# Performance work log

Measured on AMD Instinct MI355X. Metric: run time of the kernel, lower is better.

Reference implementation:

```python
import jax, jax.numpy as jnp
import numpy as np

# Dims: B=2, T=4 -> BT=8 frames; S=H*W=256 tokens/frame; L=25 stacked LLM layers; D=4096 llm hidden
BT, S, L, D = 8, 256, 25, 4096
C, NH = 1024, 8          # teacher_hid_size (hard-coded), num_heads
HD = C // NH             # 128
LAYER_IDX = np.array([24, 20, 16, 12, 8, 4, 0])  # num_layer=24 - arange(0,25,4)
J = len(LAYER_IDX)       # 7 distillation layers
SCALE = C ** -0.5        # NOTE: teacher_hid_size**-0.5, NOT head_dim**-0.5 (faithful to source)
EPS_LN, EPS_COS = 1e-5, 1e-8


def setup_inputs() -> dict:
    key = jax.random.key(0)
    ks = jax.random.split(key, 7)
    def n(k, shape, s=1.0):
        return jax.random.normal(k, shape, dtype=jnp.float32) * s
    return {
        "all_features": n(ks[0], (BT, S, L, D)),
        "teacher_features": n(ks[1], (BT, S, C)),
        "ln_gamma": jnp.ones((J, D), jnp.float32),
        "ln_beta": jnp.zeros((J, D), jnp.float32),
        "norm_w": n(ks[2], (J, C, D), 0.02),   # per-layer Linear(llm->teacher), no bias
        "input_w": n(ks[3], (C, D), 0.02),
        "input_b": n(ks[4], (C,), 0.02),
        "output_w": n(ks[5], (C, C), 0.02),
        "output_b": n(ks[6], (C,), 0.02),
    }


def reference(all_features, teacher_features, ln_gamma, ln_beta, norm_w,
              input_w, input_b, output_w, output_b):
    # Gather the distilled layers: [BT, S, J, D]
    x = all_features[:, :, LAYER_IDX]
    # Per-layer LayerNorm (each norm_layer[j] has its own affine params)
    mu = x.mean(-1, keepdims=True)
    var = ((x - mu) ** 2).mean(-1, keepdims=True)
    xn = (x - mu) * jax.lax.rsqrt(var + EPS_LN) * ln_gamma + ln_beta
    # Per-layer Linear (bias=False): stack -> vision_outputs [BT, S, J, C]
    vo = jnp.einsum('bsjd,jcd->bsjc', xn, norm_w)
    # input_layer on last hidden state: vision_input [BT, S, C]
    vin = jnp.einsum('bsd,cd->bsc', all_features[:, :, -1], input_w) + input_b
    # Hand-rolled multiplicative cross-attention over the J layer axis
    voh = vo.reshape(BT, S, J, NH, HD)
    q = voh[:, :, 0]        # [BT, S, NH, HD]
    kv = voh[:, :, 1:]      # [BT, S, J-1, NH, HD]
    scores = jnp.einsum('bshd,bskhd->bshk', q * SCALE, kv)   # [BT, S, NH, J-1]
    attn = jax.nn.softmax(scores, axis=-1)
    fuse = jnp.einsum('bshk,bskhd->bshd', attn, kv).reshape(BT, S, C)
    vf = vin + jnp.einsum('bsc,oc->bso', fuse, output_w) + output_b  # vision_feature
    # Cosine distillation loss vs teacher (torch CosineSimilarity eps=1e-8)
    na = jnp.maximum(jnp.linalg.norm(vf, axis=-1), EPS_COS)
    nb = jnp.maximum(jnp.linalg.norm(teacher_features, axis=-1), EPS_COS)
    cos = (vf * teacher_features).sum(-1) / (na * nb)        # [BT, S]
    # sum_i (1 - mean_s cos_i) / count_image, count_image = BT  ->  1 - mean over all
    return 1.0 - cos.mean()
```

## Files before the change

### kernel.cpp

```cpp
#include <hip/hip_runtime.h>
#include <cstdint>
#include <cstring>

#define M_TOK 2048
#define DDIM 4096
#define CDIM 1024
#define LTOT 25

typedef __bf16 bf16_t;
typedef __attribute__((ext_vector_type(8))) __bf16 bf16x8;
typedef __attribute__((ext_vector_type(4))) float f32x4;
typedef __attribute__((ext_vector_type(16))) float f32x16;
typedef __attribute__((ext_vector_type(8))) int i32x8;
typedef __attribute__((ext_vector_type(4))) unsigned int u32x4;
typedef unsigned char u8;

__device__ __forceinline__ void gload16(const void* g, void* l) {
  __builtin_amdgcn_global_load_lds(
      (const __attribute__((address_space(1))) unsigned int*)g,
      (__attribute__((address_space(3))) unsigned int*)l, 16, 0, 0);
}

__device__ __forceinline__ unsigned int pk4_fp8(float x, float y, float z, float w) {
  int r = __builtin_amdgcn_cvt_pk_fp8_f32(x, y, 0, false);
  r = __builtin_amdgcn_cvt_pk_fp8_f32(z, w, r, true);
  return (unsigned int)r;
}

__device__ __forceinline__ u8 f32_to_fp8(float x) {
  return (u8)(__builtin_amdgcn_cvt_pk_fp8_f32(x, 0.f, 0, false) & 0xff);
}

__device__ __forceinline__ float fp8_to_f32(u8 b) {
  return __builtin_amdgcn_cvt_f32_fp8((int)b, 0);
}

__global__ void cvt_fp8(const float* __restrict__ src, u8* __restrict__ dst, long n) {
  long stride = (long)gridDim.x * blockDim.x;
  for (long i = (long)blockIdx.x * blockDim.x + threadIdx.x; i * 8 < n; i += stride) {
    const float4* s4 = (const float4*)(src + i * 8);
    float4 a = s4[0], b = s4[1];
    uint2 pk;
    pk.x = pk4_fp8(a.x, a.y, a.z, a.w);
    pk.y = pk4_fp8(b.x, b.y, b.z, b.w);
    *(uint2*)(dst + i * 8) = pk;
  }
}

__global__ void cvt_bf16(const float* __restrict__ src, bf16_t* __restrict__ dst, long n) {
  long stride = (long)gridDim.x * blockDim.x;
  for (long i = (long)blockIdx.x * blockDim.x + threadIdx.x; i * 8 < n; i += stride) {
    const float4* s4 = (const float4*)(src + i * 8);
    float4 a = s4[0], b = s4[1];
    bf16_t o[8] = {(bf16_t)a.x, (bf16_t)a.y, (bf16_t)a.z, (bf16_t)a.w,
                   (bf16_t)b.x, (bf16_t)b.y, (bf16_t)b.z, (bf16_t)b.w};
    uint4 pk;
    __builtin_memcpy(&pk, o, 16);
    *(uint4*)(dst + i * 8) = pk;
  }
}

__global__ __launch_bounds__(256)
void ln_convert(const float* __restrict__ af, const float* __restrict__ gamma,
                const float* __restrict__ beta, u8* __restrict__ xn,
                int jBase, int fuse7)
{
  int m = blockIdx.x;
  int jl = blockIdx.y;
  int j = jBase + jl;
  int layer = (j < 7) ? (24 - 4 * j) : 24;
  const float4* row4 = (const float4*)(af + ((size_t)m * LTOT + layer) * DDIM);
  int tid = threadIdx.x;
  float4 v[4];
  float s = 0.f, ss = 0.f;
#pragma unroll
  for (int i = 0; i < 4; ++i) {
    v[i] = row4[i * 256 + tid];
    s += v[i].x + v[i].y + v[i].z + v[i].w;
    ss += v[i].x * v[i].x + v[i].y * v[i].y + v[i].z * v[i].z + v[i].w * v[i].w;
  }
  int lane = tid & 63, wv = tid >> 6;
#pragma unroll
  for (int off = 32; off; off >>= 1) { s += __shfl_xor(s, off); ss += __shfl_xor(ss, off); }
  __shared__ float red[8];
  if (lane == 0) { red[wv] = s; red[4 + wv] = ss; }
  __syncthreads();
  s = red[0] + red[1] + red[2] + red[3];
  ss = red[4] + red[5] + red[6] + red[7];
  float mu = 0.f, rs = 1.f;
  if (j < 7) {
    mu = s * (1.f / DDIM);
    float var = ss * (1.f / DDIM) - mu * mu;
    rs = rsqrtf(var + 1e-5f);
  }
  if (fuse7 && jl == 0) {
    u8* o7 = xn + ((size_t)7 * M_TOK + m) * DDIM;
#pragma unroll
    for (int i = 0; i < 4; ++i)
      ((unsigned int*)o7)[i * 256 + tid] = pk4_fp8(v[i].x, v[i].y, v[i].z, v[i].w);
  }
  u8* orow = xn + ((size_t)jl * M_TOK + m) * DDIM;
  int jw = (j < 7) ? j : 0;
  const float4* g4 = (const float4*)(gamma + (size_t)jw * DDIM);
  const float4* b4 = (const float4*)(beta + (size_t)jw * DDIM);
#pragma unroll
  for (int i = 0; i < 4; ++i) {
    float4 x = v[i];
    float4 ov;
    if (j < 7) {
      float4 g = g4[i * 256 + tid], bb = b4[i * 256 + tid];
      ov.x = (x.x - mu) * rs * g.x + bb.x;
      ov.y = (x.y - mu) * rs * g.y + bb.y;
      ov.z = (x.z - mu) * rs * g.z + bb.z;
      ov.w = (x.w - mu) * rs * g.w + bb.w;
    } else ov = x;
    ((unsigned int*)orow)[i * 256 + tid] = pk4_fp8(ov.x, ov.y, ov.z, ov.w);
  }
}

__global__ __launch_bounds__(256)
void prep(const float* __restrict__ af, const float* __restrict__ gamma,
          const float* __restrict__ beta, u8* __restrict__ xn,
          const float* __restrict__ norm_w, const float* __restrict__ input_w,
          const float* __restrict__ output_w, u8* __restrict__ wb8,
          bf16_t* __restrict__ owb)
{
  int tid = threadIdx.x;
  if (blockIdx.y == 7) {
    const long NW7 = (long)7 * CDIM * DDIM;
    const long NWI = (long)8 * CDIM * DDIM;
    const long TOT = NWI + (long)CDIM * CDIM;
    long stride = (long)gridDim.x * blockDim.x;
    for (long i = (long)blockIdx.x * blockDim.x + tid; i * 8 < TOT; i += stride) {
      long e = i * 8;
      const float* sp;
      if (e < NW7)      sp = norm_w + e;
      else if (e < NWI) sp = input_w + (e - NW7);
      else              sp = output_w + (e - NWI);
      const float4* s4 = (const float4*)sp;
      float4 a = s4[0], b = s4[1];
      if (e < NWI) {
        uint2 pk;
        pk.x = pk4_fp8(a.x, a.y, a.z, a.w);
        pk.y = pk4_fp8(b.x, b.y, b.z, b.w);
        *(uint2*)(wb8 + e) = pk;
      } else {
        bf16_t o[8] = {(bf16_t)a.x, (bf16_t)a.y, (bf16_t)a.z, (bf16_t)a.w,
                       (bf16_t)b.x, (bf16_t)b.y, (bf16_t)b.z, (bf16_t)b.w};
        uint4 pk;
        __builtin_memcpy(&pk, o, 16);
        *(uint4*)(owb + (e - NWI)) = pk;
      }
    }
    return;
  }
  int m = blockIdx.x;
  int jl = blockIdx.y;
  int layer = 24 - 4 * jl;
  const float4* row4 = (const float4*)(af + ((size_t)m * LTOT + layer) * DDIM);
  float4 v[4];
  float s = 0.f, ss = 0.f;
#pragma unroll
  for (int i = 0; i < 4; ++i) {
    v[i] = row4[i * 256 + tid];
    s += v[i].x + v[i].y + v[i].z + v[i].w;
    ss += v[i].x * v[i].x + v[i].y * v[i].y + v[i].z * v[i].z + v[i].w * v[i].w;
  }
  int lane = tid & 63, wv = tid >> 6;
#pragma unroll
  for (int off = 32; off; off >>= 1) { s += __shfl_xor(s, off); ss += __shfl_xor(ss, off); }
  __shared__ float red[8];
  if (lane == 0) { red[wv] = s; red[4 + wv] = ss; }
  __syncthreads();
  s = red[0] + red[1] + red[2] + red[3];
  ss = red[4] + red[5] + red[6] + red[7];
  float mu = s * (1.f / DDIM);
  float var = ss * (1.f / DDIM) - mu * mu;
  float rs = rsqrtf(var + 1e-5f);
  if (jl == 0) {
    u8* o7 = xn + ((size_t)7 * M_TOK + m) * DDIM;
#pragma unroll
    for (int i = 0; i < 4; ++i)
      ((unsigned int*)o7)[i * 256 + tid] = pk4_fp8(v[i].x, v[i].y, v[i].z, v[i].w);
  }
  u8* orow = xn + ((size_t)jl * M_TOK + m) * DDIM;
  const float4* g4 = (const float4*)(gamma + (size_t)jl * DDIM);
  const float4* b4 = (const float4*)(beta + (size_t)jl * DDIM);
#pragma unroll
  for (int i = 0; i < 4; ++i) {
    float4 x = v[i];
    float4 g = g4[i * 256 + tid], bb = b4[i * 256 + tid];
    float4 ov;
    ov.x = (x.x - mu) * rs * g.x + bb.x;
    ov.y = (x.y - mu) * rs * g.y + bb.y;
    ov.z = (x.z - mu) * rs * g.z + bb.z;
    ov.w = (x.w - mu) * rs * g.w + bb.w;
    ((unsigned int*)orow)[i * 256 + tid] = pk4_fp8(ov.x, ov.y, ov.z, ov.w);
  }
}

__global__ __launch_bounds__(512, 2)
void gemm256mx(const u8* __restrict__ A, const u8* __restrict__ B,
               u8* __restrict__ vo8, bf16_t* __restrict__ vinB,
               const float* __restrict__ bias,
               int Mm, int Nn, int Kk, int jBase, int tilesPerJ, int tilesN)
{
  __shared__ __align__(16) u8 smem[131072];
  int nb = gridDim.x;
  int bid = blockIdx.x;
  if ((nb & 7) == 0) { int cpx = nb >> 3; bid = (bid & 7) * cpx + (bid >> 3); }
  int jl = bid / tilesPerJ;
  int t0 = bid % tilesPerJ;
  int bm = t0 / tilesN, bn = t0 % tilesN;
  int jg = jBase + jl;

  const u8* Aj = A + (size_t)jl * Mm * Kk + (size_t)bm * 256 * Kk;
  const u8* Bj = B + (size_t)jl * Nn * Kk + (size_t)bn * 256 * Kk;

  int tid = threadIdx.x;
  int lane = tid & 63, wid = tid >> 6;
  int wm = wid >> 2, wn = wid & 3;

  int S = wid * 64 + lane;
  int ib_s = S >> 7;
  int s2 = S & 127;
  int lh_s = s2 >> 6;
  int s3 = s2 & 63;
  int l31_s = s3 >> 1;
  int hs = s3 & 1;
  int h_s = hs ^ ((l31_s >> 2) & 1);
  int row_s = ib_s * 32 + l31_s;
  int koff_s = lh_s * 32 + h_s * 16;
  const u8* AsrcC0 = Aj + (size_t)row_s * Kk + koff_s;
  const u8* AsrcC1 = Aj + (size_t)(128 + row_s) * Kk + koff_s;
  const u8* BsrcC0 = Bj + (size_t)row_s * Kk + koff_s;
  const u8* BsrcC1 = Bj + (size_t)(128 + row_s) * Kk + koff_s;

  int l31 = lane & 31;
  int lh = lane >> 5;
  int x16 = ((l31 >> 2) & 1) << 4;
  int loOff = lh * 1024 + l31 * 32 + x16;
  int hiOff = lh * 1024 + l31 * 32 + (16 ^ x16);
  int bBlk = (wn >> 1) * 8192 + ((wn & 1) * 2) * 2048;

  int NT = Kk >> 6;
  f32x16 acc[4][2] = {};

#define STAGE4(tt_)                                                              \
  { gload16(AsrcC0 + (size_t)(tt_) * 64, &smem[((tt_) & 3) * 16384 + wid * 1024]); \
    gload16(AsrcC1 + (size_t)(tt_) * 64, &smem[((tt_) & 3) * 16384 + 8192 + wid * 1024]); \
    gload16(BsrcC0 + (size_t)(tt_) * 64, &smem[65536 + ((tt_) & 3) * 16384 + wid * 1024]); \
    gload16(BsrcC1 + (size_t)(tt_) * 64, &smem[65536 + ((tt_) & 3) * 16384 + 8192 + wid * 1024]); }

#define BAR() asm volatile("s_barrier" ::: "memory")

  STAGE4(0);
  if (NT > 1) STAGE4(1);
  if (NT > 2) STAGE4(2);
  if (NT > 2)      asm volatile("s_waitcnt vmcnt(8)" ::: "memory");
  else if (NT > 1) asm volatile("s_waitcnt vmcnt(4)" ::: "memory");
  else             asm volatile("s_waitcnt vmcnt(0)" ::: "memory");
  BAR();

#pragma unroll 1
  for (int t = 0; t < NT; ++t) {
    const u8* Ab = &smem[(t & 3) * 16384 + wm * 8192];
    const u8* Bb = &smem[65536 + (t & 3) * 16384 + bBlk];
    i32x8 Afr[4], Bfr[2];
#pragma unroll
    for (int ib = 0; ib < 4; ++ib) {
      u32x4 lo = *(const u32x4*)(Ab + ib * 2048 + loOff);
      u32x4 hi = *(const u32x4*)(Ab + ib * 2048 + hiOff);
      Afr[ib][0] = lo[0]; Afr[ib][1] = lo[1]; Afr[ib][2] = lo[2]; Afr[ib][3] = lo[3];
      Afr[ib][4] = hi[0]; Afr[ib][5] = hi[1]; Afr[ib][6] = hi[2]; Afr[ib][7] = hi[3];
    }
#pragma unroll
    for (int jb = 0; jb < 2; ++jb) {
      u32x4 lo = *(const u32x4*)(Bb + jb * 2048 + loOff);
      u32x4 hi = *(const u32x4*)(Bb + jb * 2048 + hiOff);
      Bfr[jb][0] = lo[0]; Bfr[jb][1] = lo[1]; Bfr[jb][2] = lo[2]; Bfr[jb][3] = lo[3];
      Bfr[jb][4] = hi[0]; Bfr[jb][5] = hi[1]; Bfr[jb][6] = hi[2]; Bfr[jb][7] = hi[3];
    }
    if (t + 3 < NT) STAGE4(t + 3);
    __builtin_amdgcn_s_setprio(1);
#pragma unroll
    for (int ib = 0; ib < 4; ++ib)
#pragma unroll
      for (int jb = 0; jb < 2; ++jb)
        acc[ib][jb] = __builtin_amdgcn_mfma_scale_f32_32x32x64_f8f6f4(
            Afr[ib], Bfr[jb], acc[ib][jb], 0, 0, 0, 127, 0, 127);
    __builtin_amdgcn_s_setprio(0);
    if (t + 1 < NT) {
      asm volatile("s_waitcnt lgkmcnt(0)" ::: "memory");
      if (t + 3 < NT)      asm volatile("s_waitcnt vmcnt(8)" ::: "memory");
      else if (t + 2 < NT) asm volatile("s_waitcnt vmcnt(4)" ::: "memory");
      else                 asm volatile("s_waitcnt vmcnt(0)" ::: "memory");
      BAR();
    }
  }
#undef STAGE4
#undef BAR

  int col0 = bn * 256 + wn * 64 + l31;
  int row0 = bm * 256 + wm * 128 + lh * 4;
  if (jg == 7) {
    float bv0 = bias[col0];
    float bv1 = bias[col0 + 32];
#pragma unroll
    for (int ib = 0; ib < 4; ++ib) {
#pragma unroll
      for (int jb = 0; jb < 2; ++jb) {
        float bv = jb ? bv1 : bv0;
        int gc = col0 + jb * 32;
#pragma unroll
        for (int reg = 0; reg < 16; ++reg) {
          int gr = row0 + ib * 32 + (reg & 3) + 8 * (reg >> 2);
          vinB[(size_t)gr * Nn + gc] = (bf16_t)(acc[ib][jb][reg] + bv);
        }
      }
    }
  } else {
    u8* Cj = vo8 + (size_t)jg * Mm * Nn;
#pragma unroll
    for (int ib = 0; ib < 4; ++ib) {
#pragma unroll
      for (int jb = 0; jb < 2; ++jb) {
        int gc = col0 + jb * 32;
#pragma unroll
        for (int reg = 0; reg < 16; ++reg) {
          int gr = row0 + ib * 32 + (reg & 3) + 8 * (reg >> 2);
          Cj[(size_t)gr * Nn + gc] = f32_to_fp8(acc[ib][jb][reg]);
        }
      }
    }
  }
}

__global__ __launch_bounds__(256)
void gemm_bt_epi(const bf16_t* __restrict__ A, const bf16_t* __restrict__ B,
                 float* __restrict__ Cout, const float* __restrict__ bias,
                 const bf16_t* __restrict__ vin, int Mm, int Nn, int Kk, int tilesN)
{
  __shared__ bf16_t As[128 * 64];
  __shared__ bf16_t Bs[128 * 64];
  int bid = blockIdx.x;
  int bm = bid / tilesN, bn = bid % tilesN;
  const bf16_t* Aj = A + (size_t)bm * 128 * Kk;
  const bf16_t* Bj = B + (size_t)bn * 128 * Kk;

  int tid = threadIdx.x;
  int lane = tid & 63, wv = tid >> 6;
  int wm = wv >> 1, wn = wv & 1;

  f32x4 acc[4][4] = {};

  int srow = wv * 32 + (lane >> 3);
  int scol = (lane & 7) * 8;
  const bf16_t* Ag = Aj + (size_t)srow * Kk + scol;
  const bf16_t* Bg = Bj + (size_t)srow * Kk + scol;

  for (int kt = 0; kt < Kk; kt += 64) {
#pragma unroll
    for (int c = 0; c < 4; ++c) {
      gload16(Ag + kt + (size_t)(c * 8) * Kk, &As[(wv * 32 + c * 8) * 64]);
      gload16(Bg + kt + (size_t)(c * 8) * Kk, &Bs[(wv * 32 + c * 8) * 64]);
    }
    __syncthreads();
#pragma unroll
    for (int ks = 0; ks < 2; ++ks) {
      int ko = ks * 32 + (lane >> 4) * 8;
      bf16x8 af[4], bfr[4];
#pragma unroll
      for (int i = 0; i < 4; ++i) {
        af[i] = *(const bf16x8*)&As[(wm * 64 + i * 16 + (lane & 15)) * 64 + ko];
        bfr[i] = *(const bf16x8*)&Bs[(wn * 64 + i * 16 + (lane & 15)) * 64 + ko];
      }
#pragma unroll
      for (int i = 0; i < 4; ++i)
#pragma unroll
        for (int j2 = 0; j2 < 4; ++j2)
          acc[i][j2] = __builtin_amdgcn_mfma_f32_16x16x32_bf16(af[i], bfr[j2], acc[i][j2], 0, 0, 0);
    }
    __syncthreads();
  }

  int rowBase = bm * 128 + wm * 64 + (lane >> 4) * 4;
  int colBase = bn * 128 + wn * 64 + (lane & 15);
#pragma unroll
  for (int i = 0; i < 4; ++i) {
#pragma unroll
    for (int j2 = 0; j2 < 4; ++j2) {
      int gn = colBase + j2 * 16;
      float bv = bias[gn];
#pragma unroll
      for (int r = 0; r < 4; ++r) {
        int gm = rowBase + i * 16 + r;
        Cout[(size_t)gm * Nn + gn] = acc[i][j2][r] + bv + (float)vin[(size_t)gm * Nn + gn];
      }
    }
  }
}

__global__ __launch_bounds__(512)
void attn_fuse(const u8* __restrict__ vo8, bf16_t* __restrict__ fuse)
{
  int m = blockIdx.x;
  int h = threadIdx.x >> 6;
  int lane = threadIdx.x & 63;
  const size_t slab = (size_t)M_TOK * CDIM;
  const u8* base = vo8 + (size_t)m * CDIM + h * 128;
  float q0 = fp8_to_f32(base[lane]), q1 = fp8_to_f32(base[lane + 64]);
  float kv0[6], kv1[6], sc[6];
#pragma unroll
  for (int k = 0; k < 6; ++k) {
    const u8* kb = base + (size_t)(k + 1) * slab;
    kv0[k] = fp8_to_f32(kb[lane]); kv1[k] = fp8_to_f32(kb[lane + 64]);
    sc[k] = q0 * kv0[k] + q1 * kv1[k];
  }
#pragma unroll
  for (int k = 0; k < 6; ++k) {
#pragma unroll
    for (int off = 32; off; off >>= 1) sc[k] += __shfl_xor(sc[k], off);
    sc[k] *= 0.03125f;
  }
  float mx = sc[0];
#pragma unroll
  for (int k = 1; k < 6; ++k) mx = fmaxf(mx, sc[k]);
  float e[6], se = 0.f;
#pragma unroll
  for (int k = 0; k < 6; ++k) { e[k] = expf(sc[k] - mx); se += e[k]; }
  float inv = 1.f / se;
  float f0 = 0.f, f1 = 0.f;
#pragma unroll
  for (int k = 0; k < 6; ++k) { float w = e[k] * inv; f0 += w * kv0[k]; f1 += w * kv1[k]; }
  bf16_t* o = fuse + (size_t)m * CDIM + h * 128;
  o[lane] = (bf16_t)f0;
  o[lane + 64] = (bf16_t)f1;
}

__global__ __launch_bounds__(256)
void cos_row(const float* __restrict__ vf, const float* __restrict__ teacher, float* __restrict__ cosv)
{
  int m = blockIdx.x;
  int tid = threadIdx.x;
  float4 a = ((const float4*)(vf + (size_t)m * CDIM))[tid];
  float4 b = ((const float4*)(teacher + (size_t)m * CDIM))[tid];
  float dot = a.x * b.x + a.y * b.y + a.z * b.z + a.w * b.w;
  float na = a.x * a.x + a.y * a.y + a.z * a.z + a.w * a.w;
  float nb = b.x * b.x + b.y * b.y + b.z * b.z + b.w * b.w;
  int lane = tid & 63, wv = tid >> 6;
#pragma unroll
  for (int off = 32; off; off >>= 1) {
    dot += __shfl_xor(dot, off); na += __shfl_xor(na, off); nb += __shfl_xor(nb, off);
  }
  __shared__ float red[12];
  if (lane == 0) { red[wv] = dot; red[4 + wv] = na; red[8 + wv] = nb; }
  __syncthreads();
  if (tid == 0) {
    float d = red[0] + red[1] + red[2] + red[3];
    float x = red[4] + red[5] + red[6] + red[7];
    float y = red[8] + red[9] + red[10] + red[11];
    float den = fmaxf(sqrtf(x), 1e-8f) * fmaxf(sqrtf(y), 1e-8f);
    cosv[m] = d / den;
  }
}

__global__ __launch_bounds__(256)
void final_reduce(const float* __restrict__ cosv, float* __restrict__ out)
{
  int tid = threadIdx.x;
  float s = 0.f;
  for (int i = tid; i < M_TOK; i += 256) s += cosv[i];
  int lane = tid & 63, wv = tid >> 6;
#pragma unroll
  for (int off = 32; off; off >>= 1) s += __shfl_xor(s, off);
  __shared__ float red[4];
  if (lane == 0) red[wv] = s;
  __syncthreads();
  if (tid == 0) out[0] = 1.f - (red[0] + red[1] + red[2] + red[3]) * (1.f / M_TOK);
}

extern "C" void kernel_launch(void* const* d_in, const int* in_sizes, int n_in,
                              void* d_out, int out_size, void* d_ws, size_t ws_size,
                              hipStream_t stream)
{
  (void)in_sizes; (void)n_in; (void)out_size;
  const float* all_features = (const float*)d_in[0];
  const float* teacher = (const float*)d_in[1];
  const float* ln_gamma = (const float*)d_in[2];
  const float* ln_beta = (const float*)d_in[3];
  const float* norm_w = (const float*)d_in[4];
  const float* input_w = (const float*)d_in[5];
  const float* input_b = (const float*)d_in[6];
  const float* output_w = (const float*)d_in[7];
  const float* output_b = (const float*)d_in[8];
  float* out = (float*)d_out;
  char* ws = (char*)d_ws;

  const size_t M = M_TOK, D = DDIM, C = CDIM;
  const size_t xnB = 8 * M * D;
  const size_t wbB = 8 * C * D;
  const size_t owbB = C * C * 2;
  const size_t vo8B = 7 * M * C;
  const size_t vinB_ = M * C * 2;
  const size_t fuseB = M * C * 2;
  const size_t vfB = M * C * 4;
  const size_t cosB = M * 4;
  const size_t fastTotal = xnB + wbB + owbB + vo8B + vinB_ + fuseB + vfB + cosB;

  if (ws_size >= fastTotal) {
    u8* xn = (u8*)ws;
    u8* wb = (u8*)(ws + xnB);
    bf16_t* owb = (bf16_t*)(ws + xnB + wbB);
    u8* vo8 = (u8*)(ws + xnB + wbB + owbB);
    bf16_t* vinp = (bf16_t*)(ws + xnB + wbB + owbB + vo8B);
    bf16_t* fuse = (bf16_t*)(ws + xnB + wbB + owbB + vo8B + vinB_);
    float* vf = (float*)(ws + xnB + wbB + owbB + vo8B + vinB_ + fuseB);
    float* cosv = (float*)(ws + xnB + wbB + owbB + vo8B + vinB_ + fuseB + vfB);

    dim3 gp((unsigned)M, 8);
    prep<<<gp, 256, 0, stream>>>(all_features, ln_gamma, ln_beta, xn,
                                 norm_w, input_w, output_w, wb, owb);
    gemm256mx<<<256, 512, 0, stream>>>(xn, wb, vo8, vinp, input_b,
                                       (int)M, (int)C, (int)D, 0, 32, 4);
    attn_fuse<<<(unsigned)M, 512, 0, stream>>>(vo8, fuse);
    gemm_bt_epi<<<128, 256, 0, stream>>>(fuse, owb, vf, output_b, vinp,
                                         (int)M, (int)C, (int)C, 8);
    cos_row<<<(unsigned)M, 256, 0, stream>>>(vf, teacher, cosv);
    final_reduce<<<1, 256, 0, stream>>>(cosv, out);
  } else {
    const size_t xn1B = M * D;
    const size_t wb1B = C * D;
    u8* xn1 = (u8*)ws;
    u8* wb1 = (u8*)(ws + xn1B);
    bf16_t* owb = (bf16_t*)(ws + xn1B + wb1B);
    u8* vo8 = (u8*)(ws + xn1B + wb1B + owbB);
    bf16_t* vinp = (bf16_t*)(ws + xn1B + wb1B + owbB + vo8B);
    bf16_t* fuse = (bf16_t*)(ws + xn1B + wb1B + owbB + vo8B + vinB_);
    float* vf = (float*)(ws + xn1B + wb1B + owbB + vo8B + vinB_ + fuseB);
    float* cosv = (float*)(ws + xn1B + wb1B + owbB + vo8B + vinB_ + fuseB + vfB);

    cvt_bf16<<<512, 256, 0, stream>>>(output_w, owb, (long)(C * C));
    for (int j = 0; j < 8; ++j) {
      const float* wsrc = (j < 7) ? (norm_w + (size_t)j * C * D) : input_w;
      cvt_fp8<<<2048, 256, 0, stream>>>(wsrc, wb1, (long)(C * D));
      dim3 g1((unsigned)M, 1);
      ln_convert<<<g1, 256, 0, stream>>>(all_features, ln_gamma, ln_beta, xn1, j, 0);
      gemm256mx<<<32, 512, 0, stream>>>(xn1, wb1, vo8, vinp, input_b,
                                        (int)M, (int)C, (int)D, j, 32, 4);
    }
    attn_fuse<<<(unsigned)M, 512, 0, stream>>>(vo8, fuse);
    gemm_bt_epi<<<128, 256, 0, stream>>>(fuse, owb, vf, output_b, vinp,
                                         (int)M, (int)C, (int)C, 8);
    cos_row<<<(unsigned)M, 256, 0, stream>>>(vf, teacher, cosv);
    final_reduce<<<1, 256, 0, stream>>>(cosv, out);
  }
}
```

Measured before the change: 205.8 us.

## Switch FP8 GEMM to K=128 double-buffered tiles with XOR-swizzled LDS rows

The FP8 MFMA GEMM now loads 128-wide K tiles into two LDS buffers instead of 64-wide tiles into a 4-deep ring. Global-to-LDS loads use a row-major layout with an XOR swizzle on 16-byte chunks to avoid bank conflicts, and each tile runs two MFMA sub-steps. This halves the number of barriers and makes each global load fetch longer contiguous row segments. The cost is shallower prefetch (one tile ahead, with a full vmcnt(0) wait each iteration), which may expose more memory latency.

```diff
diff --git a/kernel.cpp b/kernel.cpp
--- a/kernel.cpp
+++ b/kernel.cpp
@@ -221,84 +221,91 @@
   int lane = tid & 63, wid = tid >> 6;
   int wm = wid >> 2, wn = wid & 3;
 
-  int S = wid * 64 + lane;
-  int ib_s = S >> 7;
-  int s2 = S & 127;
-  int lh_s = s2 >> 6;
-  int s3 = s2 & 63;
-  int l31_s = s3 >> 1;
-  int hs = s3 & 1;
-  int h_s = hs ^ ((l31_s >> 2) & 1);
-  int row_s = ib_s * 32 + l31_s;
-  int koff_s = lh_s * 32 + h_s * 16;
-  const u8* AsrcC0 = Aj + (size_t)row_s * Kk + koff_s;
-  const u8* AsrcC1 = Aj + (size_t)(128 + row_s) * Kk + koff_s;
-  const u8* BsrcC0 = Bj + (size_t)row_s * Kk + koff_s;
-  const u8* BsrcC1 = Bj + (size_t)(128 + row_s) * Kk + koff_s;
+  const u8* AsrcP[4];
+  const u8* BsrcP[4];
+  int AdOff[4], BdOff[4];
+  int pre = ((lane & 7) ^ ((lane >> 3) & 7)) * 16;
+#pragma unroll
+  for (int c = 0; c < 4; ++c) {
+    int S = wid * 4 + c;
+    int chunk = S >> 4, s16 = S & 15;
+    int row = chunk * 128 + s16 * 8 + (lane >> 3);
+    AsrcP[c] = Aj + (size_t)row * Kk + pre;
+    BsrcP[c] = Bj + (size_t)row * Kk + pre;
+    AdOff[c] = chunk * 16384 + s16 * 1024;
+    BdOff[c] = 32768 + chunk * 16384 + s16 * 1024;
+  }
 
   int l31 = lane & 31;
   int lh = lane >> 5;
-  int x16 = ((l31 >> 2) & 1) << 4;
-  int loOff = lh * 1024 + l31 * 32 + x16;
-  int hiOff = lh * 1024 + l31 * 32 + (16 ^ x16);
-  int bBlk = (wn >> 1) * 8192 + ((wn & 1) * 2) * 2048;
-
-  int NT = Kk >> 6;
+  int xk = l31 & 7;
+  int o0[2], o1[2];
+#pragma unroll
+  for (int s = 0; s < 2; ++s) {
+    o0[s] = ((s * 4 + lh * 2) ^ xk) * 16;
+    o1[s] = ((s * 4 + lh * 2 + 1) ^ xk) * 16;
+  }
+  int aRow = l31 * 128;
+  int bRowBase = (wn & 1) * 8192 + l31 * 128;
+  int aChunkOff = wm * 16384;
+  int bChunkOff = 32768 + (wn >> 1) * 16384;
+
+  int NT = Kk >> 7;
   f32x16 acc[4][2] = {};
 
-#define STAGE4(tt_)                                                              \
-  { gload16(AsrcC0 + (size_t)(tt_) * 64, &smem[((tt_) & 3) * 16384 + wid * 1024]); \
-    gload16(AsrcC1 + (size_t)(tt_) * 64, &smem[((tt_) & 3) * 16384 + 8192 + wid * 1024]); \
-    gload16(BsrcC0 + (size_t)(tt_) * 64, &smem[65536 + ((tt_) & 3) * 16384 + wid * 1024]); \
-    gload16(BsrcC1 + (size_t)(tt_) * 64, &smem[65536 + ((tt_) & 3) * 16384 + 8192 + wid * 1024]); }
+#define STAGE2(tt_, bf_)                                                         \
+  { _Pragma("unroll")                                                            \
+    for (int c_ = 0; c_ < 4; ++c_)                                               \
+      gload16(AsrcP[c_] + (size_t)(tt_) * 128, &smem[(bf_) * 65536 + AdOff[c_]]); \
+    _Pragma("unroll")                                                            \
+    for (int c_ = 0; c_ < 4; ++c_)                                               \
+      gload16(BsrcP[c_] + (size_t)(tt_) * 128, &smem[(bf_) * 65536 + BdOff[c_]]); }
 
 #define BAR() asm volatile("s_barrier" ::: "memory")
 
-  STAGE4(0);
-  if (NT > 1) STAGE4(1);
-  if (NT > 2) STAGE4(2);
-  if (NT > 2)      asm volatile("s_waitcnt vmcnt(8)" ::: "memory");
-  else if (NT > 1) asm volatile("s_waitcnt vmcnt(4)" ::: "memory");
-  else             asm volatile("s_waitcnt vmcnt(0)" ::: "memory");
+  STAGE2(0, 0);
+  asm volatile("s_waitcnt vmcnt(0)" ::: "memory");
   BAR();
 
 #pragma unroll 1
   for (int t = 0; t < NT; ++t) {
-    const u8* Ab = &smem[(t & 3) * 16384 + wm * 8192];
-    const u8* Bb = &smem[65536 + (t & 3) * 16384 + bBlk];
-    i32x8 Afr[4], Bfr[2];
-#pragma unroll
-    for (int ib = 0; ib < 4; ++ib) {
-      u32x4 lo = *(const u32x4*)(Ab + ib * 2048 + loOff);
-      u32x4 hi = *(const u32x4*)(Ab + ib * 2048 + hiOff);
-      Afr[ib][0] = lo[0]; Afr[ib][1] = lo[1]; Afr[ib][2] = lo[2]; Afr[ib][3] = lo[3];
-      Afr[ib][4] = hi[0]; Afr[ib][5] = hi[1]; Afr[ib][6] = hi[2]; Afr[ib][7] = hi[3];
-    }
-#pragma unroll
-    for (int jb = 0; jb < 2; ++jb) {
-      u32x4 lo = *(const u32x4*)(Bb + jb * 2048 + loOff);
-      u32x4 hi = *(const u32x4*)(Bb + jb * 2048 + hiOff);
-      Bfr[jb][0] = lo[0]; Bfr[jb][1] = lo[1]; Bfr[jb][2] = lo[2]; Bfr[jb][3] = lo[3];
-      Bfr[jb][4] = hi[0]; Bfr[jb][5] = hi[1]; Bfr[jb][6] = hi[2]; Bfr[jb][7] = hi[3];
-    }
-    if (t + 3 < NT) STAGE4(t + 3);
-    __builtin_amdgcn_s_setprio(1);
-#pragma unroll
-    for (int ib = 0; ib < 4; ++ib)
-#pragma unroll
-      for (int jb = 0; jb < 2; ++jb)
-        acc[ib][jb] = __builtin_amdgcn_mfma_scale_f32_32x32x64_f8f6f4(
-            Afr[ib], Bfr[jb], acc[ib][jb], 0, 0, 0, 127, 0, 127);
-    __builtin_amdgcn_s_setprio(0);
+    int bf = t & 1;
+    if (t + 1 < NT) STAGE2(t + 1, bf ^ 1);
+    const u8* Ac = &smem[bf * 65536 + aChunkOff];
+    const u8* Bc = &smem[bf * 65536 + bChunkOff];
+#pragma unroll
+    for (int s = 0; s < 2; ++s) {
+      i32x8 Afr[4], Bfr[2];
+#pragma unroll
+      for (int ib = 0; ib < 4; ++ib) {
+        u32x4 lo = *(const u32x4*)(Ac + ib * 4096 + aRow + o0[s]);
+        u32x4 hi = *(const u32x4*)(Ac + ib * 4096 + aRow + o1[s]);
+        Afr[ib][0] = lo[0]; Afr[ib][1] = lo[1]; Afr[ib][2] = lo[2]; Afr[ib][3] = lo[3];
+        Afr[ib][4] = hi[0]; Afr[ib][5] = hi[1]; Afr[ib][6] = hi[2]; Afr[ib][7] = hi[3];
+      }
+#pragma unroll
+      for (int jb = 0; jb < 2; ++jb) {
+        u32x4 lo = *(const u32x4*)(Bc + bRowBase + jb * 4096 + o0[s]);
+        u32x4 hi = *(const u32x4*)(Bc + bRowBase + jb * 4096 + o1[s]);
+        Bfr[jb][0] = lo[0]; Bfr[jb][1] = lo[1]; Bfr[jb][2] = lo[2]; Bfr[jb][3] = lo[3];
+        Bfr[jb][4] = hi[0]; Bfr[jb][5] = hi[1]; Bfr[jb][6] = hi[2]; Bfr[jb][7] = hi[3];
+      }
+      __builtin_amdgcn_s_setprio(1);
+#pragma unroll
+      for (int ib = 0; ib < 4; ++ib)
+#pragma unroll
+        for (int jb = 0; jb < 2; ++jb)
+          acc[ib][jb] = __builtin_amdgcn_mfma_scale_f32_32x32x64_f8f6f4(
+              Afr[ib], Bfr[jb], acc[ib][jb], 0, 0, 0, 127, 0, 127);
+      __builtin_amdgcn_s_setprio(0);
+    }
     if (t + 1 < NT) {
       asm volatile("s_waitcnt lgkmcnt(0)" ::: "memory");
-      if (t + 3 < NT)      asm volatile("s_waitcnt vmcnt(8)" ::: "memory");
-      else if (t + 2 < NT) asm volatile("s_waitcnt vmcnt(4)" ::: "memory");
-      else                 asm volatile("s_waitcnt vmcnt(0)" ::: "memory");
+      asm volatile("s_waitcnt vmcnt(0)" ::: "memory");
       BAR();
     }
   }
-#undef STAGE4
+#undef STAGE2
 #undef BAR
 
   int col0 = bn * 256 + wn * 64 + l31;
```

After: 204.6 us. Within noise of the previous version (-0.6%).
